# Optimization experiments

Hardware: AMD Instinct MI355X
Metric: run time of the kernel (lower is better)

Reference implementation:

```python
import jax, jax.numpy as jnp
import numpy as np

LEARNING_RATE = 0.1  # obj.learning_rate


def setup_inputs() -> dict:
    key = jax.random.key(0)
    k1, k2, k3, k4 = jax.random.split(key, 4)
    B, F = 50000, 100
    n_stages, n_classes, depth = 200, 10, 6
    T = n_stages * n_classes          # 2000 trees total
    n_internal = 2**depth - 1         # 63
    n_leaves = 2**depth               # 64
    x = jax.random.normal(k1, (B, F), dtype=jnp.float32)
    thresholds = jax.random.normal(k2, (T, n_internal), dtype=jnp.float32)
    leaf_values = jax.random.normal(k3, (T, n_leaves), dtype=jnp.float32)
    features = jax.random.randint(k4, (T, n_internal), 0, F, dtype=jnp.int32)
    classes = jnp.arange(n_classes, dtype=jnp.int64)
    return {"x": x, "thresholds": thresholds, "leaf_values": leaf_values,
            "features": features, "classes": classes}


def reference(x, thresholds, leaf_values, features, classes):
    # FIL-style batched traversal of complete depth-d trees.
    # Node i's children are 2i+1 (x[f] <= thr) and 2i+2 (x[f] > thr),
    # matching sklearn decision-tree split semantics.
    B = x.shape[0]
    T, n_internal = thresholds.shape
    n_leaves = leaf_values.shape[1]
    depth = int(np.log2(n_leaves))
    n_classes = classes.shape[0]

    tr = jnp.arange(T)[None, :]                      # [1, T] tree ids
    idx = jnp.zeros((B, T), dtype=jnp.int32)         # current node per (sample, tree)
    for _ in range(depth):                           # fixed small unroll (tree depth)
        f = features[tr, idx]                        # [B, T] split feature ids
        t = thresholds[tr, idx]                      # [B, T] split thresholds
        xv = jnp.take_along_axis(x, f, axis=1)       # [B, T] gathered feature values
        idx = 2 * idx + 1 + (xv > t).astype(jnp.int32)
    leaf = idx - (n_leaves - 1)                      # [B, T] leaf index in [0, n_leaves)
    vals = leaf_values[tr, leaf]                     # [B, T] per-tree outputs

    # stages-major layout: tree t = stage*n_classes + class; sum stages * lr
    # (init_ == 'zero' -> init output is zeros)
    decisions = LEARNING_RATE * vals.reshape(B, -1, n_classes).sum(axis=1)  # [B, C]
    # deviance, multiclass: predict_log_proba = log_softmax(decision_function)
    log_proba = jax.nn.log_softmax(decisions, axis=-1)
    # forward() = predict() = classes[argmax proba]; we return the float
    # log-probabilities (the differentiable hot path); argmax/class lookup is
    # a trivial epilogue: classes[jnp.argmax(log_proba, -1)]
    return log_proba
```

## Files before the change

kernel.cpp:

```cpp
#include <hip/hip_runtime.h>

#define B_SAMPLES 50000
#define F_FEATS   100
#define T_TREES   2000
#define N_INTERNAL 63
#define N_LEAVES  64
#define DEPTH     6
#define N_CLASSES 10
#define LR        0.1f

#define BLK 128
#define TREES_PER_GROUP 40
#define NCHUNK 10
#define TREES_PER_CHUNK (T_TREES / NCHUNK)
#define GROUPS_PER_CHUNK (TREES_PER_CHUNK / TREES_PER_GROUP)
#define NODE_STRIDE 64
#define NSB ((B_SAMPLES + BLK - 1) / BLK)

__global__ __launch_bounds__(256) void pack_nodes_kernel(
    const float* __restrict__ thresholds,
    const int*   __restrict__ features,
    int2*        __restrict__ nodes)
{
    int e = blockIdx.x * 256 + threadIdx.x;
    if (e < T_TREES * N_INTERNAL) {
        int t = e / N_INTERNAL;
        int i = e - t * N_INTERNAL;
        nodes[t * NODE_STRIDE + i] = make_int2(features[e], __float_as_int(thresholds[e]));
    }
}

template<bool PARTIALS>
__global__ __launch_bounds__(BLK, 2) void forest_kernel(
    const float* __restrict__ x,
    const int2*  __restrict__ nodes,
    const float* __restrict__ leaves,
    float*       __restrict__ accum)
{
    __shared__ float xs[F_FEATS * BLK];
    const int tid   = threadIdx.x;
    const int chunk = blockIdx.x % NCHUNK;
    const int sb    = blockIdx.x / NCHUNK;
    const int b     = sb * BLK + tid;
    const bool valid = (b < B_SAMPLES);

    {
        const float4* xrow = reinterpret_cast<const float4*>(x + (size_t)b * F_FEATS);
        #pragma unroll
        for (int k = 0; k < F_FEATS / 4; ++k) {
            float4 v = valid ? xrow[k] : make_float4(0.f, 0.f, 0.f, 0.f);
            xs[(4 * k + 0) * BLK + tid] = v.x;
            xs[(4 * k + 1) * BLK + tid] = v.y;
            xs[(4 * k + 2) * BLK + tid] = v.z;
            xs[(4 * k + 3) * BLK + tid] = v.w;
        }
    }
    __syncthreads();

    float acc[N_CLASSES];
    #pragma unroll
    for (int c = 0; c < N_CLASSES; ++c) acc[c] = 0.f;

    const int2*  cnodes  = nodes  + (size_t)chunk * TREES_PER_CHUNK * NODE_STRIDE;
    const float* cleaves = leaves + (size_t)chunk * TREES_PER_CHUNK * N_LEAVES;

    for (int g = 0; g < GROUPS_PER_CHUNK; ++g) {
        const int2*  nbase = cnodes  + (size_t)g * TREES_PER_GROUP * NODE_STRIDE;
        const float* lbase = cleaves + (size_t)g * TREES_PER_GROUP * N_LEAVES;

        int idx[TREES_PER_GROUP];
        #pragma unroll
        for (int j = 0; j < TREES_PER_GROUP; ++j) idx[j] = 0;

        #pragma unroll
        for (int lvl = 0; lvl < DEPTH; ++lvl) {
            int2 nd[TREES_PER_GROUP];
            #pragma unroll
            for (int j = 0; j < TREES_PER_GROUP; ++j)
                nd[j] = nbase[j * NODE_STRIDE + idx[j]];
            #pragma unroll
            for (int j = 0; j < TREES_PER_GROUP; ++j) {
                float xv  = xs[nd[j].x * BLK + tid];
                float thr = __int_as_float(nd[j].y);
                idx[j] = 2 * idx[j] + 1 + (xv > thr ? 1 : 0);
            }
        }
        #pragma unroll
        for (int j = 0; j < TREES_PER_GROUP; ++j) {
            float lv = lbase[j * N_LEAVES + (idx[j] - (N_LEAVES - 1))];
            acc[j % N_CLASSES] += lv;
        }
    }

    if (valid) {
        if (PARTIALS) {
            float2* p = reinterpret_cast<float2*>(
                accum + ((size_t)chunk * B_SAMPLES + b) * N_CLASSES);
            #pragma unroll
            for (int c = 0; c < N_CLASSES / 2; ++c)
                p[c] = make_float2(acc[2 * c], acc[2 * c + 1]);
        } else {
            #pragma unroll
            for (int c = 0; c < N_CLASSES; ++c)
                atomicAdd(&accum[(size_t)b * N_CLASSES + c], acc[c]);
        }
    }
}

template<bool PARTIALS>
__global__ __launch_bounds__(256) void softmax_kernel(
    const float* __restrict__ accum,
    float*       __restrict__ out)
{
    int b = blockIdx.x * 256 + threadIdx.x;
    if (b >= B_SAMPLES) return;

    float d[N_CLASSES];
    #pragma unroll
    for (int c = 0; c < N_CLASSES; ++c) d[c] = 0.f;

    if (PARTIALS) {
        for (int ch = 0; ch < NCHUNK; ++ch) {
            const float2* p = reinterpret_cast<const float2*>(
                accum + ((size_t)ch * B_SAMPLES + b) * N_CLASSES);
            #pragma unroll
            for (int c = 0; c < N_CLASSES / 2; ++c) {
                float2 v = p[c];
                d[2 * c]     += v.x;
                d[2 * c + 1] += v.y;
            }
        }
    } else {
        #pragma unroll
        for (int c = 0; c < N_CLASSES; ++c)
            d[c] = accum[(size_t)b * N_CLASSES + c];
    }

    #pragma unroll
    for (int c = 0; c < N_CLASSES; ++c) d[c] *= LR;
    float m = d[0];
    #pragma unroll
    for (int c = 1; c < N_CLASSES; ++c) m = fmaxf(m, d[c]);
    float ssum = 0.f;
    #pragma unroll
    for (int c = 0; c < N_CLASSES; ++c) ssum += expf(d[c] - m);
    float lse = logf(ssum);

    float2* o = reinterpret_cast<float2*>(out + (size_t)b * N_CLASSES);
    #pragma unroll
    for (int c = 0; c < N_CLASSES / 2; ++c)
        o[c] = make_float2(d[2 * c] - m - lse, d[2 * c + 1] - m - lse);
}

extern "C" void kernel_launch(void* const* d_in, const int* in_sizes, int n_in,
                              void* d_out, int out_size, void* d_ws, size_t ws_size,
                              hipStream_t stream) {
    const float* x          = (const float*)d_in[0];
    const float* thresholds = (const float*)d_in[1];
    const float* leaves     = (const float*)d_in[2];
    const int*   features   = (const int*)d_in[3];

    const size_t nodes_bytes    = (size_t)T_TREES * NODE_STRIDE * sizeof(int2);
    const size_t partials_bytes = (size_t)NCHUNK * B_SAMPLES * N_CLASSES * sizeof(float);
    const size_t accum_bytes    = (size_t)B_SAMPLES * N_CLASSES * sizeof(float);

    int2*  nodes  = (int2*)d_ws;
    float* accbuf = (float*)((char*)d_ws + nodes_bytes);
    const bool use_partials = (ws_size >= nodes_bytes + partials_bytes);

    {
        int total = T_TREES * N_INTERNAL;
        pack_nodes_kernel<<<(total + 255) / 256, 256, 0, stream>>>(thresholds, features, nodes);
    }

    if (use_partials) {
        forest_kernel<true><<<NSB * NCHUNK, BLK, 0, stream>>>(x, nodes, leaves, accbuf);
        softmax_kernel<true><<<(B_SAMPLES + 255) / 256, 256, 0, stream>>>(accbuf, (float*)d_out);
    } else {
        hipMemsetAsync(accbuf, 0, accum_bytes, stream);
        forest_kernel<false><<<NSB * NCHUNK, BLK, 0, stream>>>(x, nodes, leaves, accbuf);
        softmax_kernel<false><<<(B_SAMPLES + 255) / 256, 256, 0, stream>>>(accbuf, (float*)d_out);
    }
}
```

Baseline: 428.9 us.

## Pack sibling node pairs and speculatively prefetch both children per level

Tree nodes are repacked so each int4 holds both children of a node. Traversal loads the pair for the next level before the current comparison resolves, which takes the dependent node fetch off the critical path; the last level likewise loads both candidate leaves as one float2. Group size drops from 40 to 20 trees and launch bounds change to one block per SIMD. The cost is extra shared-memory reads for the unused child's feature and higher register pressure.

```diff
diff --git a/kernel.cpp b/kernel.cpp
--- a/kernel.cpp
+++ b/kernel.cpp
@@ -10,30 +10,41 @@
 #define LR        0.1f
 
 #define BLK 128
-#define TREES_PER_GROUP 40
+#define TPG 20
 #define NCHUNK 10
 #define TREES_PER_CHUNK (T_TREES / NCHUNK)
-#define GROUPS_PER_CHUNK (TREES_PER_CHUNK / TREES_PER_GROUP)
-#define NODE_STRIDE 64
+#define GROUPS_PER_CHUNK (TREES_PER_CHUNK / TPG)
+#define CP_STRIDE 32
 #define NSB ((B_SAMPLES + BLK - 1) / BLK)
 
 __global__ __launch_bounds__(256) void pack_nodes_kernel(
     const float* __restrict__ thresholds,
     const int*   __restrict__ features,
-    int2*        __restrict__ nodes)
+    int4*        __restrict__ cpairs)
 {
     int e = blockIdx.x * 256 + threadIdx.x;
-    if (e < T_TREES * N_INTERNAL) {
-        int t = e / N_INTERNAL;
-        int i = e - t * N_INTERNAL;
-        nodes[t * NODE_STRIDE + i] = make_int2(features[e], __float_as_int(thresholds[e]));
-    }
-}
+    int t = e >> 5, i = e & 31;
+    if (t < T_TREES) {
+        int4 v;
+        if (i < 31) {
+            int a = t * N_INTERNAL + 2 * i + 1;
+            v = make_int4(features[a],     __float_as_int(thresholds[a]),
+                          features[a + 1], __float_as_int(thresholds[a + 1]));
+        } else {
+            int r = t * N_INTERNAL;
+            v = make_int4(features[r], __float_as_int(thresholds[r]), 0, 0);
+        }
+        cpairs[t * CP_STRIDE + i] = v;
+    }
+}
+
+#define I2F __int_as_float
+#define XS(f) xs[((f) << 7) + tid]
 
 template<bool PARTIALS>
-__global__ __launch_bounds__(BLK, 2) void forest_kernel(
+__global__ __launch_bounds__(BLK, 1) void forest_kernel(
     const float* __restrict__ x,
-    const int2*  __restrict__ nodes,
+    const int4*  __restrict__ cpairs,
     const float* __restrict__ leaves,
     float*       __restrict__ accum)
 {
@@ -61,34 +72,81 @@
     #pragma unroll
     for (int c = 0; c < N_CLASSES; ++c) acc[c] = 0.f;
 
-    const int2*  cnodes  = nodes  + (size_t)chunk * TREES_PER_CHUNK * NODE_STRIDE;
-    const float* cleaves = leaves + (size_t)chunk * TREES_PER_CHUNK * N_LEAVES;
-
+    const int4*  ccp = cpairs + (size_t)chunk * TREES_PER_CHUNK * CP_STRIDE;
+    const float* clv = leaves + (size_t)chunk * TREES_PER_CHUNK * N_LEAVES;
+
+    #pragma unroll 1
     for (int g = 0; g < GROUPS_PER_CHUNK; ++g) {
-        const int2*  nbase = cnodes  + (size_t)g * TREES_PER_GROUP * NODE_STRIDE;
-        const float* lbase = cleaves + (size_t)g * TREES_PER_GROUP * N_LEAVES;
-
-        int idx[TREES_PER_GROUP];
-        #pragma unroll
-        for (int j = 0; j < TREES_PER_GROUP; ++j) idx[j] = 0;
-
-        #pragma unroll
-        for (int lvl = 0; lvl < DEPTH; ++lvl) {
-            int2 nd[TREES_PER_GROUP];
-            #pragma unroll
-            for (int j = 0; j < TREES_PER_GROUP; ++j)
-                nd[j] = nbase[j * NODE_STRIDE + idx[j]];
-            #pragma unroll
-            for (int j = 0; j < TREES_PER_GROUP; ++j) {
-                float xv  = xs[nd[j].x * BLK + tid];
-                float thr = __int_as_float(nd[j].y);
-                idx[j] = 2 * idx[j] + 1 + (xv > thr ? 1 : 0);
+        const int4*  cpb = ccp + (size_t)g * TPG * CP_STRIDE;
+        const float* lvb = clv + (size_t)g * TPG * N_LEAVES;
+
+        int   idx[TPG];
+        float thrL[TPG], thrR[TPG], xvL[TPG], xvR[TPG];
+        int4  cpt[TPG];
+
+        int2  rt[TPG]; float xv0[TPG];
+        #pragma unroll
+        for (int j = 0; j < TPG; ++j) {
+            rt[j] = *reinterpret_cast<const int2*>(cpb + j * CP_STRIDE + 31);
+        }
+        #pragma unroll
+        for (int j = 0; j < TPG; ++j) cpt[j] = cpb[j * CP_STRIDE + 0];
+        #pragma unroll
+        for (int j = 0; j < TPG; ++j) xv0[j] = XS(rt[j].x);
+        #pragma unroll
+        for (int j = 0; j < TPG; ++j) {
+            int c = xv0[j] > I2F(rt[j].y);
+            idx[j] = 1 + c;
+        }
+        #pragma unroll
+        for (int j = 0; j < TPG; ++j) {
+            thrL[j] = I2F(cpt[j].y); thrR[j] = I2F(cpt[j].w);
+            xvL[j]  = XS(cpt[j].x);  xvR[j]  = XS(cpt[j].z);
+        }
+        #pragma unroll
+        for (int j = 0; j < TPG; ++j) cpt[j] = cpb[j * CP_STRIDE + idx[j]];
+
+        float2 lf[TPG];
+
+        #pragma unroll
+        for (int lvl = 1; lvl <= 4; ++lvl) {
+            #pragma unroll
+            for (int j = 0; j < TPG; ++j) {
+                bool odd  = (idx[j] & 1);
+                float thr = odd ? thrL[j] : thrR[j];
+                float xv  = odd ? xvL[j]  : xvR[j];
+                int c = xv > thr;
+                idx[j] = 2 * idx[j] + 1 + c;
             }
-        }
-        #pragma unroll
-        for (int j = 0; j < TREES_PER_GROUP; ++j) {
-            float lv = lbase[j * N_LEAVES + (idx[j] - (N_LEAVES - 1))];
-            acc[j % N_CLASSES] += lv;
+            if (lvl < 4) {
+                #pragma unroll
+                for (int j = 0; j < TPG; ++j) {
+                    thrL[j] = I2F(cpt[j].y); thrR[j] = I2F(cpt[j].w);
+                    xvL[j]  = XS(cpt[j].x);  xvR[j]  = XS(cpt[j].z);
+                }
+                #pragma unroll
+                for (int j = 0; j < TPG; ++j) cpt[j] = cpb[j * CP_STRIDE + idx[j]];
+            } else {
+                #pragma unroll
+                for (int j = 0; j < TPG; ++j) {
+                    thrL[j] = I2F(cpt[j].y); thrR[j] = I2F(cpt[j].w);
+                    xvL[j]  = XS(cpt[j].x);  xvR[j]  = XS(cpt[j].z);
+                }
+                #pragma unroll
+                for (int j = 0; j < TPG; ++j) {
+                    lf[j] = *reinterpret_cast<const float2*>(
+                        lvb + j * N_LEAVES + (2 * idx[j] - 62));
+                }
+            }
+        }
+
+        #pragma unroll
+        for (int j = 0; j < TPG; ++j) {
+            bool odd  = (idx[j] & 1);
+            float thr = odd ? thrL[j] : thrR[j];
+            float xv  = odd ? xvL[j]  : xvR[j];
+            bool c = xv > thr;
+            acc[j % N_CLASSES] += c ? lf[j].y : lf[j].x;
         }
     }
 
@@ -160,25 +218,25 @@
     const float* leaves     = (const float*)d_in[2];
     const int*   features   = (const int*)d_in[3];
 
-    const size_t nodes_bytes    = (size_t)T_TREES * NODE_STRIDE * sizeof(int2);
+    const size_t cpairs_bytes   = (size_t)T_TREES * CP_STRIDE * sizeof(int4);
     const size_t partials_bytes = (size_t)NCHUNK * B_SAMPLES * N_CLASSES * sizeof(float);
     const size_t accum_bytes    = (size_t)B_SAMPLES * N_CLASSES * sizeof(float);
 
-    int2*  nodes  = (int2*)d_ws;
-    float* accbuf = (float*)((char*)d_ws + nodes_bytes);
-    const bool use_partials = (ws_size >= nodes_bytes + partials_bytes);
+    int4*  cpairs = (int4*)d_ws;
+    float* accbuf = (float*)((char*)d_ws + cpairs_bytes);
+    const bool use_partials = (ws_size >= cpairs_bytes + partials_bytes);
 
     {
-        int total = T_TREES * N_INTERNAL;
-        pack_nodes_kernel<<<(total + 255) / 256, 256, 0, stream>>>(thresholds, features, nodes);
+        int total = T_TREES * CP_STRIDE;
+        pack_nodes_kernel<<<(total + 255) / 256, 256, 0, stream>>>(thresholds, features, cpairs);
     }
 
     if (use_partials) {
-        forest_kernel<true><<<NSB * NCHUNK, BLK, 0, stream>>>(x, nodes, leaves, accbuf);
+        forest_kernel<true><<<NSB * NCHUNK, BLK, 0, stream>>>(x, cpairs, leaves, accbuf);
         softmax_kernel<true><<<(B_SAMPLES + 255) / 256, 256, 0, stream>>>(accbuf, (float*)d_out);
     } else {
         hipMemsetAsync(accbuf, 0, accum_bytes, stream);
-        forest_kernel<false><<<NSB * NCHUNK, BLK, 0, stream>>>(x, nodes, leaves, accbuf);
+        forest_kernel<false><<<NSB * NCHUNK, BLK, 0, stream>>>(x, cpairs, leaves, accbuf);
         softmax_kernel<false><<<(B_SAMPLES + 255) / 256, 256, 0, stream>>>(accbuf, (float*)d_out);
     }
 }
```

Result: faster. 411.2 us (-4.1%).
